# Performance work log

Hardware: AMD Instinct MI355X
Metric: run time of the kernel (lower is better)

The kernel has to match this reference:

```python
import jax, jax.numpy as jnp
import numpy as np

L, H, P = 16384, 512, 512
DT_MIN, DT_MAX = 1e-3, 1e-1


def setup_inputs() -> dict:
    key = jax.random.key(0)
    ks = jax.random.split(key, 9)
    u = jax.random.normal(ks[0], (L, H), dtype=jnp.float32)
    # stable diagonal state matrix: Re(Lambda) < 0 (HiPPO-style init)
    Lambda_re = -(0.5 * jax.random.uniform(ks[1], (P,), dtype=jnp.float32) + 1e-3)
    Lambda_im = jnp.pi * jax.random.normal(ks[2], (P,), dtype=jnp.float32)
    # lecun-normal-ish scaling for B (fan-in H) and C (fan-in P)
    B_re = jax.random.normal(ks[3], (P, H), dtype=jnp.float32) / jnp.sqrt(2.0 * H)
    B_im = jax.random.normal(ks[4], (P, H), dtype=jnp.float32) / jnp.sqrt(2.0 * H)
    C_re = jax.random.normal(ks[5], (H, P), dtype=jnp.float32) / jnp.sqrt(2.0 * P)
    C_im = jax.random.normal(ks[6], (H, P), dtype=jnp.float32) / jnp.sqrt(2.0 * P)
    D = jax.random.uniform(ks[7], (H,), dtype=jnp.float32)
    # init_log_steps: uniform in [log(dt_min), log(dt_max)]
    lo, hi = np.log(DT_MIN), np.log(DT_MAX)
    log_step = jax.random.uniform(ks[8], (P,), dtype=jnp.float32, minval=lo, maxval=hi)
    return {"u": u, "Lambda_re": Lambda_re, "Lambda_im": Lambda_im,
            "B_re": B_re, "B_im": B_im, "C_re": C_re, "C_im": C_im,
            "D": D, "log_step": log_step}


def _binary_op(q_i, q_j):
    # associative combine for diagonal linear recurrence (elementwise over (L, P))
    A_i, b_i = q_i
    A_j, b_j = q_j
    return (A_j * A_i, A_j * b_i + b_j)


def reference(u, Lambda_re, Lambda_im, B_re, B_im, C_re, C_im, D, log_step):
    Lambda = Lambda_re + 1j * Lambda_im            # (P,) complex64
    B_tilde = B_re + 1j * B_im                     # (P, H)
    C_tilde = C_re + 1j * C_im                     # (H, P)
    step = jnp.exp(log_step)                       # (P,)
    # zero-order-hold discretization
    Lambda_bar = jnp.exp(Lambda * step)            # (P,)
    B_bar = ((Lambda_bar - 1.0) / Lambda)[:, None] * B_tilde  # (P, H)
    # Bu_t = B_bar @ u_t for all t, as one GEMM: (L, H) @ (H, P)
    Bu = u.astype(B_bar.dtype) @ B_bar.T           # (L, P) complex
    Lambda_el = jnp.broadcast_to(Lambda_bar, Bu.shape)  # (L, P)
    _, xs = jax.lax.associative_scan(_binary_op, (Lambda_el, Bu))  # xs: (L, P)
    # y_t = Re(C_tilde @ x_t) + D * u_t, batched as one GEMM
    ys = (xs @ C_tilde.T).real + D * u             # (L, H)
    return ys.astype(jnp.float32)
```

## Files before the change

### kernel.cpp

```cpp
#include <hip/hip_runtime.h>
#include <stdint.h>

#define L_DIM 16384
#define H_DIM 512
#define P_DIM 512
#define T_CH  64
#define NC    (L_DIM / T_CH)
#define LP    ((size_t)L_DIM * P_DIM)
#define LH    ((size_t)L_DIM * H_DIM)
#define NCP   ((size_t)NC * P_DIM)

typedef unsigned short u16;
typedef __attribute__((ext_vector_type(8))) _Float16 f16x8;
typedef __attribute__((ext_vector_type(4))) float f32x4;
typedef __attribute__((ext_vector_type(8))) unsigned short u16x8;

__device__ __forceinline__ u16 f2h(float x) {
    _Float16 h = (_Float16)x;
    return __builtin_bit_cast(u16, h);
}
__device__ __forceinline__ float h2f(u16 h) {
    return (float)__builtin_bit_cast(_Float16, h);
}

__device__ __forceinline__ void gload16(const void* g, void* lds) {
    __builtin_amdgcn_global_load_lds(
        (const __attribute__((address_space(1))) void*)g,
        (__attribute__((address_space(3))) void*)(uintptr_t)lds,
        16, 0, 0);
}

__device__ __forceinline__ f32x4 mfma_f16(f16x8 a, f16x8 b, f32x4 c) {
    return __builtin_amdgcn_mfma_f32_16x16x32_f16(a, b, c, 0, 0, 0);
}

__global__ __launch_bounds__(P_DIM) void prep_kernel(
    const float* __restrict__ Lre, const float* __restrict__ Lim,
    const float* __restrict__ log_step,
    float* __restrict__ lbr, float* __restrict__ lbi,
    float* __restrict__ l64r, float* __restrict__ l64i,
    float* __restrict__ gre, float* __restrict__ gim)
{
    int p = threadIdx.x;
    float st = expf(log_step[p]);
    float ar = Lre[p] * st, ai = Lim[p] * st;
    float er = expf(ar);
    float lr = er * cosf(ai), li = er * sinf(ai);
    lbr[p] = lr; lbi[p] = li;
    float den = Lre[p] * Lre[p] + Lim[p] * Lim[p];
    float x = lr - 1.0f, y = li;
    gre[p] = (x * Lre[p] + y * Lim[p]) / den;
    gim[p] = (y * Lre[p] - x * Lim[p]) / den;
    float pr = 1.f, pi2 = 0.f;
    for (int k = 0; k < T_CH; ++k) {
        float nr = pr * lr - pi2 * li;
        float ni = pr * li + pi2 * lr;
        pr = nr; pi2 = ni;
    }
    l64r[p] = pr; l64i[p] = pi2;
}

__global__ __launch_bounds__(256) void convert_u(
    const float* __restrict__ u, u16* __restrict__ uh)
{
    size_t i = ((size_t)blockIdx.x * 256 + threadIdx.x) * 8;
    float4 v0 = *(const float4*)(u + i);
    float4 v1 = *(const float4*)(u + i + 4);
    u16x8 h;
    h[0] = f2h(v0.x); h[1] = f2h(v0.y); h[2] = f2h(v0.z); h[3] = f2h(v0.w);
    h[4] = f2h(v1.x); h[5] = f2h(v1.y); h[6] = f2h(v1.z); h[7] = f2h(v1.w);
    *(u16x8*)(uh + i) = h;
}

__global__ __launch_bounds__(256) void build_bcat(
    const float* __restrict__ Bre, const float* __restrict__ Bim,
    const float* __restrict__ gre, const float* __restrict__ gim,
    u16* __restrict__ Bcat)
{
    int idx = blockIdx.x * 256 + threadIdx.x;
    int p = idx >> 9, h = idx & 511;
    float br = Bre[idx], bi = Bim[idx];
    float gr = gre[p], gi = gim[p];
    float vr = gr * br - gi * bi;
    float vi = gr * bi + gi * br;
    Bcat[(size_t)p * 512 + h]         = f2h(vr);
    Bcat[(size_t)(512 + p) * 512 + h] = f2h(vi);
}

__global__ __launch_bounds__(256) void build_ccat(
    const float* __restrict__ Cre, const float* __restrict__ Cim,
    u16* __restrict__ Ccat)
{
    int idx = blockIdx.x * 256 + threadIdx.x;
    int h = idx >> 9, p = idx & 511;
    size_t row = (size_t)h * 1024;
    Ccat[row + p]       = f2h(Cre[idx]);
    Ccat[row + 512 + p] = f2h(-Cim[idx]);
}

template<int KTOT, int NBN, int MODE>
__global__ __launch_bounds__(256, 2) void gemm_mfma(
    const u16* __restrict__ A0, const u16* __restrict__ A1,
    const u16* __restrict__ Bmat,
    void* __restrict__ O0v, void* __restrict__ O1v,
    const float* __restrict__ Dvec, const u16* __restrict__ uIn)
{
    __shared__ u16 Als[128 * 64];
    __shared__ u16 Bls[128 * 64];

    const u16* Aseg[2] = {A0, A1};

    int b = blockIdx.x;
    int m = (b & 7) * 16 + b / (8 * NBN);
    int n = (b >> 3) & (NBN - 1);
    int m0 = m * 128, n0 = n * 128;

    int tid = threadIdx.x;
    int w = tid >> 6, lane = tid & 63;
    int wm = w >> 1, wn = w & 1;

    f32x4 acc[4][4];
    #pragma unroll
    for (int i = 0; i < 4; ++i)
        #pragma unroll
        for (int j = 0; j < 4; ++j) acc[i][j] = (f32x4)0.f;

    int lr8  = lane >> 3;
    int slin = lane & 7;

    char* AlsB = (char*)&Als[0];
    char* BlsB = (char*)&Bls[0];

    const int NSEG = KTOT / 512;
    #pragma unroll
    for (int seg = 0; seg < NSEG; ++seg) {
        const u16* Ap = Aseg[seg];
        for (int k8 = 0; k8 < 8; ++k8) {
            int ko = k8 * 64;
            int kB = seg * 512 + ko;

            __syncthreads();
            #pragma unroll
            for (int c = 0; c < 4; ++c) {
                int sidx = w * 4 + c;
                int r = sidx * 8 + lr8;
                int g = slin ^ (r & 7);
                const u16* ga = Ap + (size_t)(m0 + r) * 512 + ko + g * 8;
                gload16(ga, AlsB + sidx * 1024);
                const u16* gb = Bmat + (size_t)(n0 + r) * KTOT + kB + g * 8;
                gload16(gb, BlsB + sidx * 1024);
            }
            asm volatile("s_waitcnt vmcnt(0)" ::: "memory");
            __syncthreads();

            f16x8 a[4][2], bf[4][2];
            #pragma unroll
            for (int mm = 0; mm < 4; ++mm)
                #pragma unroll
                for (int kk = 0; kk < 2; ++kk) {
                    int row = wm * 64 + mm * 16 + (lane & 15);
                    int sl  = kk * 4 + (lane >> 4);
                    int off = row * 128 + ((sl ^ (lane & 7)) << 4);
                    a[mm][kk] = *(const f16x8*)(AlsB + off);
                }
            #pragma unroll
            for (int nn = 0; nn < 4; ++nn)
                #pragma unroll
                for (int kk = 0; kk < 2; ++kk) {
                    int row = wn * 64 + nn * 16 + (lane & 15);
                    int sl  = kk * 4 + (lane >> 4);
                    int off = row * 128 + ((sl ^ (lane & 7)) << 4);
                    bf[nn][kk] = *(const f16x8*)(BlsB + off);
                }
            #pragma unroll
            for (int mm = 0; mm < 4; ++mm)
                #pragma unroll
                for (int nn = 0; nn < 4; ++nn) {
                    acc[mm][nn] = mfma_f16(a[mm][0], bf[nn][0], acc[mm][nn]);
                    acc[mm][nn] = mfma_f16(a[mm][1], bf[nn][1], acc[mm][nn]);
                }
        }
    }

    int colb = n0 + wn * 64;
    int rowb = m0 + wm * 64;
    #pragma unroll
    for (int mm = 0; mm < 4; ++mm)
        #pragma unroll
        for (int nn = 0; nn < 4; ++nn) {
            f32x4 v = acc[mm][nn];
            int col = colb + nn * 16 + (lane & 15);
            #pragma unroll
            for (int j = 0; j < 4; ++j) {
                int row = rowb + mm * 16 + (lane >> 4) * 4 + j;
                if (MODE == 0) {
                    size_t oidx = (size_t)row * 512 + (col & 511);
                    u16 hv = f2h(v[j]);
                    if (col < 512) ((u16*)O0v)[oidx] = hv;
                    else           ((u16*)O1v)[oidx] = hv;
                } else {
                    size_t oidx = (size_t)row * 512 + col;
                    ((float*)O0v)[oidx] = v[j] + Dvec[col] * h2f(uIn[oidx]);
                }
            }
        }
}

__global__ __launch_bounds__(P_DIM) void scan_sums(
    const u16* __restrict__ burh, const u16* __restrict__ buih,
    const float* __restrict__ lbr, const float* __restrict__ lbi,
    float* __restrict__ bcr, float* __restrict__ bci)
{
    int p = threadIdx.x;
    int c = blockIdx.x;
    float lr = lbr[p], li = lbi[p];
    float xr = 0.f, xi = 0.f;
    size_t base = (size_t)c * T_CH * P_DIM + p;
    #pragma unroll 8
    for (int k = 0; k < T_CH; ++k) {
        size_t idx = base + (size_t)k * P_DIM;
        float br = h2f(burh[idx]), bi = h2f(buih[idx]);
        float nr = fmaf(lr, xr, fmaf(-li, xi, br));
        float ni = fmaf(lr, xi, fmaf( li, xr, bi));
        xr = nr; xi = ni;
    }
    bcr[(size_t)c * P_DIM + p] = xr;
    bci[(size_t)c * P_DIM + p] = xi;
}

__global__ __launch_bounds__(P_DIM) void scan_chunks(
    const float* __restrict__ bcr, const float* __restrict__ bci,
    const float* __restrict__ l64r, const float* __restrict__ l64i,
    float* __restrict__ carr, float* __restrict__ cari)
{
    int p = threadIdx.x;
    float lr = l64r[p], li = l64i[p];
    float sr = 0.f, si = 0.f;
    #pragma unroll 8
    for (int c = 0; c < NC; ++c) {
        size_t idx = (size_t)c * P_DIM + p;
        carr[idx] = sr; cari[idx] = si;
        float br = bcr[idx], bi = bci[idx];
        float nr = fmaf(lr, sr, fmaf(-li, si, br));
        float ni = fmaf(lr, si, fmaf( li, sr, bi));
        sr = nr; si = ni;
    }
}

__global__ __launch_bounds__(P_DIM) void scan_fix(
    const u16* __restrict__ burh, const u16* __restrict__ buih,
    const float* __restrict__ lbr, const float* __restrict__ lbi,
    const float* __restrict__ carr, const float* __restrict__ cari,
    u16* __restrict__ xrh, u16* __restrict__ xih)
{
    int p = threadIdx.x;
    int c = blockIdx.x;
    float lr = lbr[p], li = lbi[p];
    float xr = carr[(size_t)c * P_DIM + p];
    float xi = cari[(size_t)c * P_DIM + p];
    size_t base = (size_t)c * T_CH * P_DIM + p;
    #pragma unroll 4
    for (int k = 0; k < T_CH; ++k) {
        size_t idx = base + (size_t)k * P_DIM;
        float br = h2f(burh[idx]), bi = h2f(buih[idx]);
        float nr = fmaf(lr, xr, fmaf(-li, xi, br));
        float ni = fmaf(lr, xi, fmaf( li, xr, bi));
        xr = nr; xi = ni;
        xrh[idx] = f2h(xr);
        xih[idx] = f2h(xi);
    }
}

extern "C" void kernel_launch(void* const* d_in, const int* in_sizes, int n_in,
                              void* d_out, int out_size, void* d_ws, size_t ws_size,
                              hipStream_t stream)
{
    const float* u        = (const float*)d_in[0];
    const float* Lre      = (const float*)d_in[1];
    const float* Lim      = (const float*)d_in[2];
    const float* Bre      = (const float*)d_in[3];
    const float* Bim      = (const float*)d_in[4];
    const float* Cre      = (const float*)d_in[5];
    const float* Cim      = (const float*)d_in[6];
    const float* D        = (const float*)d_in[7];
    const float* log_step = (const float*)d_in[8];
    float* out = (float*)d_out;

    char* w8 = (char*)d_ws;
    u16*   burh = (u16*)(w8);
    u16*   buih = (u16*)(w8 + 16777216);
    u16*   xrh  = (u16*)(w8 + 33554432);
    u16*   xih  = (u16*)(w8 + 50331648);
    u16*   uh   = (u16*)(w8 + 67108864);
    u16*   Bcat = (u16*)(w8 + 83886080);
    u16*   Ccat = (u16*)(w8 + 84934656);
    float* bcr  = (float*)(w8 + 85983232);
    float* bci  = bcr + NCP;
    float* carr = bci + NCP;
    float* cari = carr + NCP;
    float* lbr  = cari + NCP;
    float* lbi  = lbr + P_DIM;
    float* l64r = lbi + P_DIM;
    float* l64i = l64r + P_DIM;
    float* gre  = l64i + P_DIM;
    float* gim  = gre + P_DIM;

    prep_kernel<<<1, P_DIM, 0, stream>>>(Lre, Lim, log_step, lbr, lbi, l64r, l64i, gre, gim);
    convert_u<<<(int)(LH / 2048), 256, 0, stream>>>(u, uh);
    build_bcat<<<(P_DIM * H_DIM) / 256, 256, 0, stream>>>(Bre, Bim, gre, gim, Bcat);
    build_ccat<<<(H_DIM * P_DIM) / 256, 256, 0, stream>>>(Cre, Cim, Ccat);

    gemm_mfma<512, 8, 0><<<1024, 256, 0, stream>>>(
        uh, uh, Bcat, burh, buih, nullptr, nullptr);

    scan_sums<<<NC, P_DIM, 0, stream>>>(burh, buih, lbr, lbi, bcr, bci);
    scan_chunks<<<1, P_DIM, 0, stream>>>(bcr, bci, l64r, l64i, carr, cari);
    scan_fix<<<NC, P_DIM, 0, stream>>>(burh, buih, lbr, lbi, carr, cari, xrh, xih);

    gemm_mfma<1024, 4, 1><<<512, 256, 0, stream>>>(
        xrh, xih, Ccat, out, nullptr, D, uh);
}
```

Before: 124.8 us.

## Fuse chunk-sum computation into Bu GEMM epilogue via precomputed lambda powers

```diff
diff --git a/kernel.cpp b/kernel.cpp
--- a/kernel.cpp
+++ b/kernel.cpp
@@ -4,11 +4,10 @@
 #define L_DIM 16384
 #define H_DIM 512
 #define P_DIM 512
-#define T_CH  64
+#define T_CH  32
 #define NC    (L_DIM / T_CH)
 #define LP    ((size_t)L_DIM * P_DIM)
 #define LH    ((size_t)L_DIM * H_DIM)
-#define NCP   ((size_t)NC * P_DIM)
 
 typedef unsigned short u16;
 typedef __attribute__((ext_vector_type(8))) _Float16 f16x8;
@@ -38,8 +37,8 @@
     const float* __restrict__ Lre, const float* __restrict__ Lim,
     const float* __restrict__ log_step,
     float* __restrict__ lbr, float* __restrict__ lbi,
-    float* __restrict__ l64r, float* __restrict__ l64i,
-    float* __restrict__ gre, float* __restrict__ gim)
+    float* __restrict__ gre, float* __restrict__ gim,
+    float* __restrict__ powr, float* __restrict__ powi)
 {
     int p = threadIdx.x;
     float st = expf(log_step[p]);
@@ -52,12 +51,14 @@
     gre[p] = (x * Lre[p] + y * Lim[p]) / den;
     gim[p] = (y * Lre[p] - x * Lim[p]) / den;
     float pr = 1.f, pi2 = 0.f;
-    for (int k = 0; k < T_CH; ++k) {
+    powr[p] = 1.f; powi[p] = 0.f;
+    for (int k = 1; k <= T_CH; ++k) {
         float nr = pr * lr - pi2 * li;
         float ni = pr * li + pi2 * lr;
         pr = nr; pi2 = ni;
-    }
-    l64r[p] = pr; l64i[p] = pi2;
+        powr[(size_t)k * P_DIM + p] = pr;
+        powi[(size_t)k * P_DIM + p] = pi2;
+    }
 }
 
 __global__ __launch_bounds__(256) void convert_u(
@@ -81,10 +82,8 @@
     int p = idx >> 9, h = idx & 511;
     float br = Bre[idx], bi = Bim[idx];
     float gr = gre[p], gi = gim[p];
-    float vr = gr * br - gi * bi;
-    float vi = gr * bi + gi * br;
-    Bcat[(size_t)p * 512 + h]         = f2h(vr);
-    Bcat[(size_t)(512 + p) * 512 + h] = f2h(vi);
+    Bcat[(size_t)p * 512 + h]         = f2h(gr * br - gi * bi);
+    Bcat[(size_t)(512 + p) * 512 + h] = f2h(gr * bi + gi * br);
 }
 
 __global__ __launch_bounds__(256) void build_ccat(
@@ -103,7 +102,10 @@
     const u16* __restrict__ A0, const u16* __restrict__ A1,
     const u16* __restrict__ Bmat,
     void* __restrict__ O0v, void* __restrict__ O1v,
-    const float* __restrict__ Dvec, const u16* __restrict__ uIn)
+    const float* __restrict__ Dvec, const u16* __restrict__ uIn,
+    const float* __restrict__ powr, const float* __restrict__ powi,
+    float* __restrict__ Rwr, float* __restrict__ Rwi,
+    float* __restrict__ Iwr, float* __restrict__ Iwi)
 {
     __shared__ u16 Als[128 * 64];
     __shared__ u16 Bls[128 * 64];
@@ -193,7 +195,7 @@
             #pragma unroll
             for (int j = 0; j < 4; ++j) {
                 int row = rowb + mm * 16 + (lane >> 4) * 4 + j;
-                if (MODE == 0) {
+                if constexpr (MODE == 0) {
                     size_t oidx = (size_t)row * 512 + (col & 511);
                     u16 hv = f2h(v[j]);
                     if (col < 512) ((u16*)O0v)[oidx] = hv;
@@ -204,45 +206,75 @@
                 }
             }
         }
-}
-
-__global__ __launch_bounds__(P_DIM) void scan_sums(
-    const u16* __restrict__ burh, const u16* __restrict__ buih,
-    const float* __restrict__ lbr, const float* __restrict__ lbi,
-    float* __restrict__ bcr, float* __restrict__ bci)
-{
-    int p = threadIdx.x;
-    int c = blockIdx.x;
-    float lr = lbr[p], li = lbi[p];
-    float xr = 0.f, xi = 0.f;
-    size_t base = (size_t)c * T_CH * P_DIM + p;
-    #pragma unroll 8
-    for (int k = 0; k < T_CH; ++k) {
-        size_t idx = base + (size_t)k * P_DIM;
-        float br = h2f(burh[idx]), bi = h2f(buih[idx]);
-        float nr = fmaf(lr, xr, fmaf(-li, xi, br));
-        float ni = fmaf(lr, xi, fmaf( li, xr, bi));
-        xr = nr; xi = ni;
-    }
-    bcr[(size_t)c * P_DIM + p] = xr;
-    bci[(size_t)c * P_DIM + p] = xi;
-}
-
-__global__ __launch_bounds__(P_DIM) void scan_chunks(
-    const float* __restrict__ bcr, const float* __restrict__ bci,
-    const float* __restrict__ l64r, const float* __restrict__ l64i,
+
+    if constexpr (MODE == 0) {
+        float swr[2][4] = {{0.f}};
+        float swi[2][4] = {{0.f}};
+        #pragma unroll
+        for (int mm = 0; mm < 4; ++mm) {
+            int ch = mm >> 1;
+            #pragma unroll
+            for (int nn = 0; nn < 4; ++nn) {
+                int col = colb + nn * 16 + (lane & 15);
+                int p = col & 511;
+                f32x4 v = acc[mm][nn];
+                #pragma unroll
+                for (int j = 0; j < 4; ++j) {
+                    int k = (mm & 1) * 16 + (lane >> 4) * 4 + j;
+                    int e = (T_CH - 1) - k;
+                    float wr = powr[(size_t)e * 512 + p];
+                    float wi = powi[(size_t)e * 512 + p];
+                    swr[ch][nn] = fmaf(wr, v[j], swr[ch][nn]);
+                    swi[ch][nn] = fmaf(wi, v[j], swi[ch][nn]);
+                }
+            }
+        }
+        #pragma unroll
+        for (int ch = 0; ch < 2; ++ch)
+            #pragma unroll
+            for (int nn = 0; nn < 4; ++nn) {
+                float a2 = swr[ch][nn];
+                a2 += __shfl_xor(a2, 16); a2 += __shfl_xor(a2, 32);
+                swr[ch][nn] = a2;
+                float b2 = swi[ch][nn];
+                b2 += __shfl_xor(b2, 16); b2 += __shfl_xor(b2, 32);
+                swi[ch][nn] = b2;
+            }
+        if (lane < 16) {
+            #pragma unroll
+            for (int ch = 0; ch < 2; ++ch) {
+                int c = (m0 >> 5) + wm * 2 + ch;
+                #pragma unroll
+                for (int nn = 0; nn < 4; ++nn) {
+                    int col = colb + nn * 16 + lane;
+                    int p = col & 511;
+                    size_t pidx = (size_t)c * 512 + p;
+                    if (col < 512) { Rwr[pidx] = swr[ch][nn]; Rwi[pidx] = swi[ch][nn]; }
+                    else           { Iwr[pidx] = swr[ch][nn]; Iwi[pidx] = swi[ch][nn]; }
+                }
+            }
+        }
+    }
+}
+
+__global__ __launch_bounds__(64) void scan_chunks(
+    const float* __restrict__ Rwr, const float* __restrict__ Rwi,
+    const float* __restrict__ Iwr, const float* __restrict__ Iwi,
+    const float* __restrict__ powr, const float* __restrict__ powi,
     float* __restrict__ carr, float* __restrict__ cari)
 {
-    int p = threadIdx.x;
-    float lr = l64r[p], li = l64i[p];
+    int p = blockIdx.x * 64 + threadIdx.x;
+    float ar = powr[(size_t)T_CH * P_DIM + p];
+    float ai = powi[(size_t)T_CH * P_DIM + p];
     float sr = 0.f, si = 0.f;
     #pragma unroll 8
     for (int c = 0; c < NC; ++c) {
         size_t idx = (size_t)c * P_DIM + p;
         carr[idx] = sr; cari[idx] = si;
-        float br = bcr[idx], bi = bci[idx];
-        float nr = fmaf(lr, sr, fmaf(-li, si, br));
-        float ni = fmaf(lr, si, fmaf( li, sr, bi));
+        float vre = Rwr[idx] - Iwi[idx];
+        float vim = Rwi[idx] + Iwr[idx];
+        float nr = fmaf(ar, sr, fmaf(-ai, si, vre));
+        float ni = fmaf(ar, si, fmaf( ai, sr, vim));
         sr = nr; si = ni;
     }
 }
@@ -294,29 +326,32 @@
     u16*   uh   = (u16*)(w8 + 67108864);
     u16*   Bcat = (u16*)(w8 + 83886080);
     u16*   Ccat = (u16*)(w8 + 84934656);
-    float* bcr  = (float*)(w8 + 85983232);
-    float* bci  = bcr + NCP;
-    float* carr = bci + NCP;
-    float* cari = carr + NCP;
-    float* lbr  = cari + NCP;
+    float* Rwr  = (float*)(w8 + 85983232);
+    float* Rwi  = (float*)(w8 + 87031808);
+    float* Iwr  = (float*)(w8 + 88080384);
+    float* Iwi  = (float*)(w8 + 89128960);
+    float* carr = (float*)(w8 + 90177536);
+    float* cari = (float*)(w8 + 91226112);
+    float* powr = (float*)(w8 + 92274688);
+    float* powi = (float*)(w8 + 92342272);
+    float* lbr  = (float*)(w8 + 92409856);
     float* lbi  = lbr + P_DIM;
-    float* l64r = lbi + P_DIM;
-    float* l64i = l64r + P_DIM;
-    float* gre  = l64i + P_DIM;
+    float* gre  = lbi + P_DIM;
     float* gim  = gre + P_DIM;
 
-    prep_kernel<<<1, P_DIM, 0, stream>>>(Lre, Lim, log_step, lbr, lbi, l64r, l64i, gre, gim);
+    prep_kernel<<<1, P_DIM, 0, stream>>>(Lre, Lim, log_step, lbr, lbi, gre, gim, powr, powi);
     convert_u<<<(int)(LH / 2048), 256, 0, stream>>>(u, uh);
     build_bcat<<<(P_DIM * H_DIM) / 256, 256, 0, stream>>>(Bre, Bim, gre, gim, Bcat);
     build_ccat<<<(H_DIM * P_DIM) / 256, 256, 0, stream>>>(Cre, Cim, Ccat);
 
     gemm_mfma<512, 8, 0><<<1024, 256, 0, stream>>>(
-        uh, uh, Bcat, burh, buih, nullptr, nullptr);
-
-    scan_sums<<<NC, P_DIM, 0, stream>>>(burh, buih, lbr, lbi, bcr, bci);
-    scan_chunks<<<1, P_DIM, 0, stream>>>(bcr, bci, l64r, l64i, carr, cari);
+        uh, uh, Bcat, burh, buih, nullptr, nullptr,
+        powr, powi, Rwr, Rwi, Iwr, Iwi);
+
+    scan_chunks<<<8, 64, 0, stream>>>(Rwr, Rwi, Iwr, Iwi, powr, powi, carr, cari);
     scan_fix<<<NC, P_DIM, 0, stream>>>(burh, buih, lbr, lbi, carr, cari, xrh, xih);
 
     gemm_mfma<1024, 4, 1><<<512, 256, 0, stream>>>(
-        xrh, xih, Ccat, out, nullptr, D, uh);
-}
+        xrh, xih, Ccat, out, nullptr, D, uh,
+        nullptr, nullptr, nullptr, nullptr, nullptr, nullptr);
+}
```

Result: slower. 130.6 us (+4.7%).
